# Optimization experiments

Hardware: AMD Instinct MI355X
Metric: run time of the kernel (lower is better)

Reference implementation:

```python
import jax, jax.numpy as jnp
import numpy as np


def setup_inputs() -> dict:
    key = jax.random.key(0)
    k1, k2 = jax.random.split(key)
    B, N, M, D = 8, 4096, 4096, 3
    pred_points = jax.random.normal(k1, (B, N, D), dtype=jnp.float32)
    gt_points = jax.random.normal(k2, (B, M, D), dtype=jnp.float32)
    return {"pred_points": pred_points, "gt_points": gt_points}


def _chamfer_l2(pred, gt):
    # pytorch3d chamfer_distance with norm=2 uses SQUARED euclidean distances.
    x2 = jnp.sum(pred * pred, axis=-1)            # [B, N]
    y2 = jnp.sum(gt * gt, axis=-1)                # [B, M]
    xy = jnp.einsum('bnd,bmd->bnm', pred, gt)     # [B, N, M]
    d = x2[:, :, None] + y2[:, None, :] - 2.0 * xy
    d = jnp.maximum(d, 0.0)  # numerical safety
    cham_x = jnp.mean(jnp.min(d, axis=2), axis=1)  # mean over N, per batch
    cham_y = jnp.mean(jnp.min(d, axis=1), axis=1)  # mean over M, per batch
    # batch_reduction='mean', loss = cham_x + cham_y
    return jnp.mean(cham_x) + jnp.mean(cham_y)


def reference(pred_points, gt_points):
    return _chamfer_l2(pred_points.astype(jnp.float32), gt_points.astype(jnp.float32))
```

## Files before the change

### kernel.cpp

```cpp
#include <hip/hip_runtime.h>


#define CH_B     8
#define CH_NPTS  4096
#define CH_NQ    (2 * CH_B * CH_NPTS)
#define CH_NCH   4
#define CH_CHUNK (CH_NPTS / CH_NCH)


__global__ __launch_bounds__(256) void chamfer_pack(
    const float* __restrict__ pred, const float* __restrict__ gt,
    float4* __restrict__ packed, float* __restrict__ out)
{
    const int i = blockIdx.x * 256 + threadIdx.x;
    if (i == 0) out[0] = 0.0f;
    const int p = i & (CH_B * CH_NPTS - 1);
    const float* src = (i >> 15) ? gt : pred;
    const float x = src[p * 3 + 0];
    const float y = src[p * 3 + 1];
    const float z = src[p * 3 + 2];
    packed[i] = make_float4(x, y, z, fmaf(x, x, fmaf(y, y, z * z)));
}

__global__ __launch_bounds__(256) void chamfer_main(
    const float4* __restrict__ packed, float* __restrict__ partial)
{
    const int g     = blockIdx.x;
    const int chunk = g & 3;
    const int rest  = g >> 2;
    const int dir   = rest & 1;
    const int b     = (rest >> 1) & 7;
    const int tile  = rest >> 4;

    const float4* qcloud = packed + (size_t)dir * (CH_B * CH_NPTS) + b * CH_NPTS;
    const float4* tcloud = packed + (size_t)(dir ^ 1) * (CH_B * CH_NPTS) + b * CH_NPTS;

    const int q = tile * 256 + threadIdx.x;
    const float4 Q = qcloud[q];
    const float qx2 = -2.0f * Q.x;
    const float qy2 = -2.0f * Q.y;
    const float qz2 = -2.0f * Q.z;

    const float4* __restrict__ t = tcloud + chunk * CH_CHUNK;

    const float INF = 3.4028235e38f;
    float m0 = INF, m1 = INF, m2 = INF, m3 = INF;

    for (int j = 0; j < CH_CHUNK; j += 8) {
        float e[8];
        #pragma unroll
        for (int k = 0; k < 8; ++k) {
            const float4 T = t[j + k];
            e[k] = fmaf(qx2, T.x, fmaf(qy2, T.y, fmaf(qz2, T.z, T.w)));
        }
        m0 = fminf(m0, fminf(e[0], e[1]));
        m1 = fminf(m1, fminf(e[2], e[3]));
        m2 = fminf(m2, fminf(e[4], e[5]));
        m3 = fminf(m3, fminf(e[6], e[7]));
    }
    const float m = fminf(fminf(m0, m1), fminf(m2, m3));

    partial[chunk * CH_NQ + dir * (CH_B * CH_NPTS) + b * CH_NPTS + q] = m;
}

__global__ __launch_bounds__(256) void chamfer_reduce(
    const float4* __restrict__ packed, const float* __restrict__ partial,
    float* __restrict__ out)
{
    __shared__ float wsum[4];
    const int i = blockIdx.x * 256 + threadIdx.x;

    float m = fminf(fminf(partial[i],             partial[CH_NQ + i]),
                    fminf(partial[2 * CH_NQ + i], partial[3 * CH_NQ + i]));
    const float q2 = packed[i].w;
    const float d  = fmaxf(q2 + m, 0.0f);

    float s = d * (1.0f / (8.0f * 4096.0f));
    #pragma unroll
    for (int off = 32; off > 0; off >>= 1)
        s += __shfl_down(s, off);

    const int lane = threadIdx.x & 63;
    const int wid  = threadIdx.x >> 6;
    if (lane == 0) wsum[wid] = s;
    __syncthreads();
    if (threadIdx.x == 0)
        atomicAdd(out, wsum[0] + wsum[1] + wsum[2] + wsum[3]);
}

extern "C" void kernel_launch(void* const* d_in, const int* in_sizes, int n_in,
                              void* d_out, int out_size, void* d_ws, size_t ws_size,
                              hipStream_t stream) {
    const float* pred = (const float*)d_in[0];
    const float* gt   = (const float*)d_in[1];
    float* out        = (float*)d_out;

    float4* packed  = (float4*)d_ws;
    float*  partial = (float*)((char*)d_ws + (size_t)CH_NQ * 16);

    chamfer_pack  <<<CH_NQ / 256, 256, 0, stream>>>(pred, gt, packed, out);
    chamfer_main  <<<CH_NCH * 256, 256, 0, stream>>>(packed, partial);
    chamfer_reduce<<<CH_NQ / 256, 256, 0, stream>>>(packed, partial, out);
}
```

Before: 101.8 us.

## Fuse reduce into main kernel via atomicMin and last-block ticket

Removes the separate reduce kernel. Each block now keeps two queries per thread and splits the targets into 8 chunks. It publishes partial minima through an order-preserving float-to-uint atomicMin, and the last block of each group, found by a ticket counter, does the final sum. This saves one launch and halves target loads per query, since each loaded target is reused for two queries. The cost is global atomics, threadfences and a serialized tail in the last block.

Result: slower. 137.2 us (+34.8%).

```diff
diff --git a/kernel.cpp b/kernel.cpp
--- a/kernel.cpp
+++ b/kernel.cpp
@@ -1,20 +1,34 @@
 #include <hip/hip_runtime.h>
 
 
-#define CH_B     8
-#define CH_NPTS  4096
-#define CH_NQ    (2 * CH_B * CH_NPTS)
-#define CH_NCH   4
-#define CH_CHUNK (CH_NPTS / CH_NCH)
+#define CH_NPTS   4096
+#define CH_HALF   32768
+#define CH_NQ     65536
+#define CH_C      8
+#define CH_TGT    (CH_NPTS / CH_C)
+#define CH_GROUPS 128
+#define CH_QPB    512
+
+__device__ __forceinline__ unsigned fl2u(float f) {
+    unsigned b = __float_as_uint(f);
+    return (b & 0x80000000u) ? ~b : (b | 0x80000000u);
+}
+__device__ __forceinline__ float u2fl(unsigned u) {
+    unsigned b = (u & 0x80000000u) ? (u ^ 0x80000000u) : ~u;
+    return __uint_as_float(b);
+}
 
 
 __global__ __launch_bounds__(256) void chamfer_pack(
     const float* __restrict__ pred, const float* __restrict__ gt,
-    float4* __restrict__ packed, float* __restrict__ out)
+    float4* __restrict__ packed, unsigned* __restrict__ mins,
+    unsigned* __restrict__ ticket, float* __restrict__ out)
 {
     const int i = blockIdx.x * 256 + threadIdx.x;
     if (i == 0) out[0] = 0.0f;
-    const int p = i & (CH_B * CH_NPTS - 1);
+    if (i < CH_GROUPS) ticket[i] = 0u;
+    mins[i] = 0xFFFFFFFFu;
+    const int p = i & (CH_HALF - 1);
     const float* src = (i >> 15) ? gt : pred;
     const float x = src[p * 3 + 0];
     const float y = src[p * 3 + 1];
@@ -23,68 +37,75 @@
 }
 
 __global__ __launch_bounds__(256) void chamfer_main(
-    const float4* __restrict__ packed, float* __restrict__ partial)
+    const float4* __restrict__ packed, unsigned* __restrict__ mins,
+    unsigned* __restrict__ ticket, float* __restrict__ out)
 {
-    const int g     = blockIdx.x;
-    const int chunk = g & 3;
-    const int rest  = g >> 2;
-    const int dir   = rest & 1;
-    const int b     = (rest >> 1) & 7;
-    const int tile  = rest >> 4;
+    const int tid   = threadIdx.x;
+    const int group = blockIdx.x >> 3;
+    const int chunk = blockIdx.x & 7;
+    const int dir   = group >> 6;
+    const int b     = (group >> 3) & 7;
 
-    const float4* qcloud = packed + (size_t)dir * (CH_B * CH_NPTS) + b * CH_NPTS;
-    const float4* tcloud = packed + (size_t)(dir ^ 1) * (CH_B * CH_NPTS) + b * CH_NPTS;
+    const int qa = group * CH_QPB + tid;
+    const int qb = qa + 256;
+    const float4 Qa = packed[qa];
+    const float4 Qb = packed[qb];
+    const float ax = -2.f * Qa.x, ay = -2.f * Qa.y, az = -2.f * Qa.z;
+    const float bx = -2.f * Qb.x, by = -2.f * Qb.y, bz = -2.f * Qb.z;
 
-    const int q = tile * 256 + threadIdx.x;
-    const float4 Q = qcloud[q];
-    const float qx2 = -2.0f * Q.x;
-    const float qy2 = -2.0f * Q.y;
-    const float qz2 = -2.0f * Q.z;
-
-    const float4* __restrict__ t = tcloud + chunk * CH_CHUNK;
+    const float4* __restrict__ t =
+        packed + (dir ^ 1) * CH_HALF + b * CH_NPTS + chunk * CH_TGT;
 
     const float INF = 3.4028235e38f;
-    float m0 = INF, m1 = INF, m2 = INF, m3 = INF;
+    float mA0 = INF, mA1 = INF, mB0 = INF, mB1 = INF;
 
-    for (int j = 0; j < CH_CHUNK; j += 8) {
-        float e[8];
+    #pragma unroll 2
+    for (int j = 0; j < CH_TGT; j += 8) {
+        float ea[8], eb[8];
         #pragma unroll
         for (int k = 0; k < 8; ++k) {
             const float4 T = t[j + k];
-            e[k] = fmaf(qx2, T.x, fmaf(qy2, T.y, fmaf(qz2, T.z, T.w)));
+            const float tw = T.w;
+            ea[k] = fmaf(ax, T.x, fmaf(ay, T.y, fmaf(az, T.z, tw)));
+            eb[k] = fmaf(bx, T.x, fmaf(by, T.y, fmaf(bz, T.z, tw)));
         }
-        m0 = fminf(m0, fminf(e[0], e[1]));
-        m1 = fminf(m1, fminf(e[2], e[3]));
-        m2 = fminf(m2, fminf(e[4], e[5]));
-        m3 = fminf(m3, fminf(e[6], e[7]));
+        mA0 = fminf(fminf(mA0, ea[0]), ea[1]);
+        mA1 = fminf(fminf(mA1, ea[2]), ea[3]);
+        mA0 = fminf(fminf(mA0, ea[4]), ea[5]);
+        mA1 = fminf(fminf(mA1, ea[6]), ea[7]);
+        mB0 = fminf(fminf(mB0, eb[0]), eb[1]);
+        mB1 = fminf(fminf(mB1, eb[2]), eb[3]);
+        mB0 = fminf(fminf(mB0, eb[4]), eb[5]);
+        mB1 = fminf(fminf(mB1, eb[6]), eb[7]);
     }
-    const float m = fminf(fminf(m0, m1), fminf(m2, m3));
 
-    partial[chunk * CH_NQ + dir * (CH_B * CH_NPTS) + b * CH_NPTS + q] = m;
-}
+    atomicMin(&mins[qa], fl2u(fminf(mA0, mA1)));
+    atomicMin(&mins[qb], fl2u(fminf(mB0, mB1)));
 
-__global__ __launch_bounds__(256) void chamfer_reduce(
-    const float4* __restrict__ packed, const float* __restrict__ partial,
-    float* __restrict__ out)
-{
+    __shared__ int  isLast;
     __shared__ float wsum[4];
-    const int i = blockIdx.x * 256 + threadIdx.x;
+    __syncthreads();
+    if (tid == 0) {
+        __threadfence();
+        unsigned old = atomicAdd(&ticket[group], 1u);
+        isLast = (old == CH_C - 1);
+    }
+    __syncthreads();
+    if (!isLast) return;
 
-    float m = fminf(fminf(partial[i],             partial[CH_NQ + i]),
-                    fminf(partial[2 * CH_NQ + i], partial[3 * CH_NQ + i]));
-    const float q2 = packed[i].w;
-    const float d  = fmaxf(q2 + m, 0.0f);
+    __threadfence();
+    const float ma = u2fl(atomicMin(&mins[qa], 0xFFFFFFFFu));
+    const float mb = u2fl(atomicMin(&mins[qb], 0xFFFFFFFFu));
+    const float da = fmaxf(Qa.w + ma, 0.0f);
+    const float db = fmaxf(Qb.w + mb, 0.0f);
 
-    float s = d * (1.0f / (8.0f * 4096.0f));
+    float s = (da + db) * (1.0f / (8.0f * 4096.0f));
     #pragma unroll
     for (int off = 32; off > 0; off >>= 1)
         s += __shfl_down(s, off);
-
-    const int lane = threadIdx.x & 63;
-    const int wid  = threadIdx.x >> 6;
-    if (lane == 0) wsum[wid] = s;
+    if ((tid & 63) == 0) wsum[tid >> 6] = s;
     __syncthreads();
-    if (threadIdx.x == 0)
+    if (tid == 0)
         atomicAdd(out, wsum[0] + wsum[1] + wsum[2] + wsum[3]);
 }
 
@@ -95,10 +116,10 @@
     const float* gt   = (const float*)d_in[1];
     float* out        = (float*)d_out;
 
-    float4* packed  = (float4*)d_ws;
-    float*  partial = (float*)((char*)d_ws + (size_t)CH_NQ * 16);
+    float4*   packed = (float4*)d_ws;
+    unsigned* mins   = (unsigned*)((char*)d_ws + (size_t)CH_NQ * 16);
+    unsigned* ticket = (unsigned*)((char*)d_ws + (size_t)CH_NQ * 16 + (size_t)CH_NQ * 4);
 
-    chamfer_pack  <<<CH_NQ / 256, 256, 0, stream>>>(pred, gt, packed, out);
-    chamfer_main  <<<CH_NCH * 256, 256, 0, stream>>>(packed, partial);
-    chamfer_reduce<<<CH_NQ / 256, 256, 0, stream>>>(packed, partial, out);
+    chamfer_pack<<<CH_NQ / 256, 256, 0, stream>>>(pred, gt, packed, mins, ticket, out);
+    chamfer_main<<<CH_GROUPS * CH_C, 256, 0, stream>>>(packed, mins, ticket, out);
 }
```
